# Kernel tuning notes

Measured on AMD Instinct MI355X. Metric: run time of the kernel, lower is better.

## Reference

```python
import jax, jax.numpy as jnp
import numpy as np

D_MODEL = 1024
N_HEADS = 16
D_K = D_MODEL // N_HEADS  # 64
D_FF = 2688
THETA = 10000.0
EPS = 1e-5
B, S = 2, 2048


def _rmsnorm(x, w):
    xf = x.astype(jnp.float32)
    ms = jnp.mean(xf * xf, axis=-1, keepdims=True)
    return (xf * w * jax.lax.rsqrt(ms + EPS)).astype(x.dtype)


def _rope(x, cos, sin):
    # x: [B, S, H, D_K]; cos/sin: [S, D_K//2]
    xe = x[..., 0::2]
    xo = x[..., 1::2]
    c = cos[None, :, None, :]
    s = sin[None, :, None, :]
    re = xe * c - xo * s
    ro = xe * s + xo * c
    # interleave back to even/odd layout
    return jnp.stack([re, ro], axis=-1).reshape(x.shape)


def setup_inputs() -> dict:
    key = jax.random.key(0)
    ks = jax.random.split(key, 12)
    sc = 0.02  # keep activations numerically sane (stand-in for trunc_normal init)
    return {
        "x": jax.random.normal(ks[0], (B, S, D_MODEL), dtype=jnp.float32),
        "ln1_w": jax.random.normal(ks[1], (D_MODEL,), dtype=jnp.float32) * sc + 1.0,
        "q_w": jax.random.normal(ks[2], (D_MODEL, D_MODEL), dtype=jnp.float32) * sc,
        "k_w": jax.random.normal(ks[3], (D_MODEL, D_MODEL), dtype=jnp.float32) * sc,
        "v_w": jax.random.normal(ks[4], (D_MODEL, D_MODEL), dtype=jnp.float32) * sc,
        "o_w": jax.random.normal(ks[5], (D_MODEL, D_MODEL), dtype=jnp.float32) * sc,
        "ln2_w": jax.random.normal(ks[6], (D_MODEL,), dtype=jnp.float32) * sc + 1.0,
        "w1_w": jax.random.normal(ks[7], (D_FF, D_MODEL), dtype=jnp.float32) * sc,
        "w3_w": jax.random.normal(ks[8], (D_FF, D_MODEL), dtype=jnp.float32) * sc,
        "w2_w": jax.random.normal(ks[9], (D_MODEL, D_FF), dtype=jnp.float32) * sc,
        "token_positions": jnp.arange(S, dtype=jnp.int32),
    }


def reference(x, ln1_w, q_w, k_w, v_w, o_w, ln2_w, w1_w, w3_w, w2_w, token_positions):
    b, s, _ = x.shape
    # --- pre-norm attention sublayer ---
    h = _rmsnorm(x, ln1_w)
    Q = (h @ q_w.T).reshape(b, s, N_HEADS, D_K)
    K = (h @ k_w.T).reshape(b, s, N_HEADS, D_K)
    V = (h @ v_w.T).reshape(b, s, N_HEADS, D_K)

    # RoPE tables from token positions
    pos = token_positions.astype(jnp.float32)                      # [S]
    kk = jnp.arange(D_K // 2, dtype=jnp.float32)
    inv_freq = THETA ** (-2.0 * kk / D_K)                          # [D_K/2]
    ang = pos[:, None] * inv_freq[None, :]                          # [S, D_K/2]
    cos, sin = jnp.cos(ang), jnp.sin(ang)

    Qr = _rope(Q, cos, sin)
    Kr = _rope(K, cos, sin)

    scale = 1.0 / jnp.sqrt(jnp.float32(D_K))
    scores = jnp.einsum("bqhd,bkhd->bhqk", Qr, Kr) * scale          # [B,H,S,S]
    causal = jnp.tril(jnp.ones((s, s), dtype=bool))
    scores = jnp.where(causal[None, None], scores, jnp.float32(-10000.0))
    attn = jax.nn.softmax(scores, axis=-1)
    ctx = jnp.einsum("bhqk,bkhd->bqhd", attn, V).reshape(b, s, D_MODEL)
    x1 = x + ctx @ o_w.T

    # --- pre-norm SwiGLU FFN sublayer ---
    h2 = _rmsnorm(x1, ln2_w)
    g = h2 @ w1_w.T                                                 # [B,S,D_FF]
    u = h2 @ w3_w.T
    ffn = (g * jax.nn.sigmoid(g) * u) @ w2_w.T
    return x1 + ffn
```

## Files before the change

kernel.cpp:

```cpp
#include <hip/hip_runtime.h>
#include <cstdint>

#define DM   1024
#define NH   16
#define DK   64
#define DFF  2688
#define SEQ  2048
#define BB   2
#define MTOT (BB*SEQ)

typedef __attribute__((ext_vector_type(8))) short short8;
typedef __attribute__((ext_vector_type(4))) float f32x4;

typedef const __attribute__((address_space(1))) void* gaddr_t;
typedef __attribute__((address_space(3))) void* laddr_t;
#define GLOAD_LDS16(g, l) __builtin_amdgcn_global_load_lds((gaddr_t)(g), (laddr_t)(l), 16, 0, 0)
#define MFMA16(a, b, c) __builtin_amdgcn_mfma_f32_16x16x32_bf16((a), (b), (c), 0, 0, 0)
#define WAIT_LDS() __builtin_amdgcn_s_waitcnt(0xc07f)

__device__ __forceinline__ float bf2f(unsigned short u) {
    union { unsigned int i; float f; } v; v.i = ((unsigned int)u) << 16; return v.f;
}
__device__ __forceinline__ unsigned short f2bf(float f) {
    union { float f; unsigned int i; } v; v.f = f;
    unsigned int r = v.i + 0x7fffu + ((v.i >> 16) & 1u);
    return (unsigned short)(r >> 16);
}
__device__ __forceinline__ unsigned long long pack4bf(float a, float b, float c, float d) {
    return (unsigned long long)f2bf(a) | ((unsigned long long)f2bf(b) << 16)
         | ((unsigned long long)f2bf(c) << 32) | ((unsigned long long)f2bf(d) << 48);
}

__global__ __launch_bounds__(256)
void prep_k(const float* __restrict__ q_w, const float* __restrict__ k_w,
            const float* __restrict__ v_w, const float* __restrict__ o_w,
            const float* __restrict__ w1_w, const float* __restrict__ w3_w,
            const float* __restrict__ w2_w,
            unsigned short* __restrict__ Wqkv, unsigned short* __restrict__ Wo,
            unsigned short* __restrict__ W13, unsigned short* __restrict__ W2) {
    const int blk = blockIdx.x;
    const float* src; unsigned short* dst; int cols, rmul, roff, i;
    if (blk < 4096) {
        const int rr = blk >> 10;
        i = (blk & 1023) * 256 + threadIdx.x;
        cols = 1024; rmul = 1;
        if (rr == 0)      { src = q_w; dst = Wqkv; roff = 0; }
        else if (rr == 1) { src = k_w; dst = Wqkv; roff = 1024; }
        else if (rr == 2) { src = v_w; dst = Wqkv; roff = 2048; }
        else              { src = o_w; dst = Wo;   roff = 0; }
    } else if (blk < 6784) {
        i = (blk - 4096) * 256 + threadIdx.x; src = w1_w; dst = W13; cols = 1024; rmul = 2; roff = 0;
    } else if (blk < 9472) {
        i = (blk - 6784) * 256 + threadIdx.x; src = w3_w; dst = W13; cols = 1024; rmul = 2; roff = 1;
    } else {
        i = (blk - 9472) * 256 + threadIdx.x; src = w2_w; dst = W2;  cols = 2688; rmul = 1; roff = 0;
    }
    const int e = i * 4;
    const int r = e / cols, c = e - r * cols;
    const float4 v = *(const float4*)(src + e);
    ushort4 o;
    o.x = f2bf(v.x); o.y = f2bf(v.y); o.z = f2bf(v.z); o.w = f2bf(v.w);
    *(ushort4*)(dst + (size_t)(r * rmul + roff) * cols + c) = o;
}

__global__ __launch_bounds__(256)
void rmsnorm_k(const float* __restrict__ x, const float* __restrict__ w,
               unsigned short* __restrict__ out) {
    const int row = blockIdx.x;
    const int tid = threadIdx.x;
    const float4 v = ((const float4*)(x + (size_t)row * DM))[tid];
    float ss = v.x * v.x + v.y * v.y + v.z * v.z + v.w * v.w;
#pragma unroll
    for (int off = 32; off > 0; off >>= 1) ss += __shfl_down(ss, off, 64);
    __shared__ float sred[4];
    const int wave = tid >> 6, lane = tid & 63;
    if (lane == 0) sred[wave] = ss;
    __syncthreads();
    const float tot = sred[0] + sred[1] + sred[2] + sred[3];
    const float rinv = rsqrtf(tot * (1.0f / DM) + 1e-5f);
    const float4 wv = ((const float4*)w)[tid];
    ushort4 o;
    o.x = f2bf(v.x * wv.x * rinv);
    o.y = f2bf(v.y * wv.y * rinv);
    o.z = f2bf(v.z * wv.z * rinv);
    o.w = f2bf(v.w * wv.w * rinv);
    ((ushort4*)(out + (size_t)row * DM))[tid] = o;
}

template <int EPI, int TN>
__global__ __launch_bounds__(256)
void gemm_bt(const unsigned short* __restrict__ A,
             const unsigned short* __restrict__ B,
             unsigned short* __restrict__ Cb,
             float* __restrict__ Cf,
             const float* __restrict__ R,
             int N, int K) {
    constexpr int NJ  = (TN == 128) ? 4 : 2;
    constexpr int BPT = (TN == 128) ? 4 : 2;
    __shared__ unsigned short As[8192];
    __shared__ unsigned short Bs[TN * 64];
    const int tid = threadIdx.x;
    const int wave = tid >> 6, lane = tid & 63;
    const int l15 = lane & 15, quad = lane >> 4;
    const int m0 = blockIdx.y * 128, n0 = blockIdx.x * TN;
    const int wr = (TN == 128) ? (wave >> 1) * 64 : (wave & 1) * 64;
    const int wc = (TN == 128) ? (wave & 1) * 64 : (wave >> 1) * 32;

    const f32x4 z4 = {0.f, 0.f, 0.f, 0.f};
    f32x4 acc[4][NJ];
#pragma unroll
    for (int i = 0; i < 4; i++)
#pragma unroll
        for (int j = 0; j < NJ; j++) acc[i][j] = z4;

    const unsigned short* ap[4];
    int albase[4];
#pragma unroll
    for (int i = 0; i < 4; i++) {
        const int s = i * 256 + tid;
        ap[i] = A + (size_t)(m0 + (s & 127)) * K + (s >> 7) * 8;
        albase[i] = (i * 256 + wave * 64) * 8;
    }
    const unsigned short* bp[BPT];
    int blbase[BPT];
#pragma unroll
    for (int i = 0; i < BPT; i++) {
        const int s = i * 256 + tid;
        const int nn = (TN == 128) ? (s & 127) : (s & 63);
        const int k8 = (TN == 128) ? (s >> 7) : (s >> 6);
        bp[i] = B + (size_t)(n0 + nn) * K + k8 * 8;
        blbase[i] = (i * 256 + wave * 64) * 8;
    }

    const int nk = K >> 6;
    for (int kc = 0; kc < nk; kc++) {
        __syncthreads();
#pragma unroll
        for (int i = 0; i < 4; i++) { GLOAD_LDS16(ap[i], &As[albase[i]]); ap[i] += 64; }
#pragma unroll
        for (int i = 0; i < BPT; i++) { GLOAD_LDS16(bp[i], &Bs[blbase[i]]); bp[i] += 64; }
        __syncthreads();
#pragma unroll
        for (int h = 0; h < 2; h++) {
            short8 af[4], bg[NJ];
#pragma unroll
            for (int t = 0; t < 4; t++)
                af[t] = *(const short8*)(&As[((quad + 4 * h) * 128 + wr + t * 16 + l15) * 8]);
#pragma unroll
            for (int t = 0; t < NJ; t++)
                bg[t] = *(const short8*)(&Bs[((quad + 4 * h) * TN + wc + t * 16 + l15) * 8]);
#pragma unroll
            for (int i = 0; i < 4; i++)
#pragma unroll
                for (int j = 0; j < NJ; j++)
                    acc[i][j] = MFMA16(bg[j], af[i], acc[i][j]);
        }
    }

#pragma unroll
    for (int i = 0; i < 4; i++) {
        const int r = m0 + wr + i * 16 + l15;
#pragma unroll
        for (int j = 0; j < NJ; j++) {
            const int cc = n0 + wc + j * 16 + quad * 4;
            const size_t idx = (size_t)r * N + cc;
            if (EPI == 0) {
                *(unsigned long long*)(Cb + idx) =
                    pack4bf(acc[i][j][0], acc[i][j][1], acc[i][j][2], acc[i][j][3]);
            } else {
                const float4 rv = *(const float4*)(R + idx);
                float4 ov;
                ov.x = acc[i][j][0] + rv.x;
                ov.y = acc[i][j][1] + rv.y;
                ov.z = acc[i][j][2] + rv.z;
                ov.w = acc[i][j][3] + rv.w;
                *(float4*)(Cf + idx) = ov;
            }
        }
    }
}

__global__ void rope_tab_k(const int* __restrict__ pos, float* __restrict__ tab) {
    const int s = blockIdx.x, t = threadIdx.x;
    const int kk = t & 31;
    const float ang = (float)pos[s] * __expf(-0.28782313662f * (float)kk);
    tab[s * 64 + t] = (t < 32) ? cosf(ang) : sinf(ang);
}

__global__ __launch_bounds__(256)
void rope_k(const unsigned short* __restrict__ qkv, const float* __restrict__ tab,
            unsigned short* __restrict__ Qr, unsigned short* __restrict__ Kr) {
    const int m = blockIdx.x;
    const int s = m & (SEQ - 1), b = m >> 11;
    const int tid = threadIdx.x;
#pragma unroll
    for (int i = 0; i < 2; i++) {
        const int pr = i * 256 + tid;
        const int h = pr >> 5, k = pr & 31;
        const float cs = tab[s * 64 + k];
        const float sn = tab[s * 64 + 32 + k];
        const size_t so = (size_t)m * 3072 + h * 64 + 2 * k;
        const size_t doff = ((size_t)(b * NH + h) * SEQ + s) * DK + 2 * k;
        const unsigned int q2 = *(const unsigned int*)(qkv + so);
        float xe = bf2f((unsigned short)(q2 & 0xffffu));
        float xo = bf2f((unsigned short)(q2 >> 16));
        *(unsigned int*)(Qr + doff) =
            (unsigned int)f2bf(xe * cs - xo * sn) | ((unsigned int)f2bf(xe * sn + xo * cs) << 16);
        const unsigned int k2 = *(const unsigned int*)(qkv + so + 1024);
        xe = bf2f((unsigned short)(k2 & 0xffffu));
        xo = bf2f((unsigned short)(k2 >> 16));
        *(unsigned int*)(Kr + doff) =
            (unsigned int)f2bf(xe * cs - xo * sn) | ((unsigned int)f2bf(xe * sn + xo * cs) << 16);
    }
}

__global__ __launch_bounds__(256)
void vtrans_k(const unsigned short* __restrict__ qkv, unsigned short* __restrict__ Vt) {
    __shared__ unsigned short tile[64 * 72];
    const int bh = blockIdx.y;
    const int b = bh >> 4, h = bh & 15;
    const int s0 = blockIdx.x * 64;
    const int tid = threadIdx.x;
#pragma unroll
    for (int i = 0; i < 2; i++) {
        const int idx = i * 256 + tid;
        const int sl = idx >> 3, d8 = (idx & 7) * 8;
        const uint4 v = *(const uint4*)(qkv + (size_t)(b * SEQ + s0 + sl) * 3072 + 2048 + h * 64 + d8);
        *(uint4*)(tile + sl * 72 + d8) = v;
    }
    __syncthreads();
#pragma unroll
    for (int i = 0; i < 2; i++) {
        const int idx = i * 256 + tid;
        const int d = idx >> 3, s8 = (idx & 7) * 8;
        unsigned short tmp[8] __attribute__((aligned(16)));
#pragma unroll
        for (int j = 0; j < 8; j++) tmp[j] = tile[(s8 + j) * 72 + d];
        *(uint4*)(Vt + ((size_t)bh * DK + d) * SEQ + s0 + s8) = *(const uint4*)tmp;
    }
}

template <bool MASK>
__device__ __forceinline__ void softmax_tile(f32x4 st[4], float& li, unsigned short* Pw,
                                             int l15, int quad, int j0, int myq) {
    float lsum = 0.f;
#pragma unroll
    for (int t = 0; t < 4; t++) {
#pragma unroll
        for (int r = 0; r < 4; r++) {
            float v = st[t][r] * 0.125f;
            if (MASK) {
                const int key = j0 + t * 16 + quad * 4 + r;
                if (key > myq) v = -1e30f;
            }
            const float p = __expf(v);
            st[t][r] = p;
            lsum += p;
        }
        *(unsigned long long*)(Pw + l15 * 72 + t * 16 + quad * 4) =
            pack4bf(st[t][0], st[t][1], st[t][2], st[t][3]);
    }
    li += lsum;
}

__global__ __launch_bounds__(256, 2)
void attn_k(const unsigned short* __restrict__ Qr, const unsigned short* __restrict__ Kr,
            const unsigned short* __restrict__ Vt, unsigned short* __restrict__ ctx) {
    __shared__ unsigned short KVl[2][8192];
    __shared__ unsigned short Pl[4 * 2 * 1152];
    const int tid = threadIdx.x;
    const int wave = tid >> 6, lane = tid & 63;
    const int l15 = lane & 15, quad = lane >> 4;
    const int bh = blockIdx.y, b = bh >> 4, h = bh & 15;
    const int g = blockIdx.x;
    const int qtA = g * 4 + wave, qtB = 127 - qtA;
    const int q0A = qtA * 16, q0B = qtB * 16;
    const int countA = g + 1, countB = 32 - g;
    const unsigned short* Kb = Kr + (size_t)bh * SEQ * DK;
    const unsigned short* Vb = Vt + (size_t)bh * DK * SEQ;

    const unsigned short* QbA = Qr + ((size_t)bh * SEQ + q0A) * DK;
    const unsigned short* QbB = Qr + ((size_t)bh * SEQ + q0B) * DK;
    const short8 qfA0 = *(const short8*)(QbA + l15 * DK + quad * 8);
    const short8 qfA1 = *(const short8*)(QbA + l15 * DK + 32 + quad * 8);
    const short8 qfB0 = *(const short8*)(QbB + l15 * DK + quad * 8);
    const short8 qfB1 = *(const short8*)(QbB + l15 * DK + 32 + quad * 8);

    const int slot0 = wave * 128 + lane, slot1 = slot0 + 64;
    const int ck0 = slot0 >> 3, s0 = slot0 & 7;
    const int ck1 = slot1 >> 3, s1 = slot1 & 7;
    const unsigned short* kp0 = Kb + ck0 * 64 + (s0 ^ (ck0 & 7)) * 8;
    const unsigned short* kp1 = Kb + ck1 * 64 + (s1 ^ (ck1 & 7)) * 8;
    const unsigned short* vp0 = Vb + ck0 * 2048 + (s0 ^ (ck0 & 7)) * 8;
    const unsigned short* vp1 = Vb + ck1 * 2048 + (s1 ^ (ck1 & 7)) * 8;
    const int kb0 = wave * 1024, kb1 = kb0 + 512;

    unsigned short* PA = Pl + (wave * 2 + 0) * 1152;
    unsigned short* PB = Pl + (wave * 2 + 1) * 1152;

    const f32x4 z4 = {0.f, 0.f, 0.f, 0.f};
    f32x4 oA[4], oB[4];
#pragma unroll
    for (int d = 0; d < 4; d++) { oA[d] = z4; oB[d] = z4; }
    float liA = 0.f, liB = 0.f;
    const int myqA = q0A + l15, myqB = q0B + l15;
    const int xr = l15 & 7;

    GLOAD_LDS16(kp0, &KVl[0][kb0]);
    GLOAD_LDS16(kp1, &KVl[0][kb1]);
    GLOAD_LDS16(vp0, &KVl[0][4096 + kb0]);
    GLOAD_LDS16(vp1, &KVl[0][4096 + kb1]);
    kp0 += 4096; kp1 += 4096; vp0 += 64; vp1 += 64;

    for (int j = 0; j < countB; ++j) {
        const int bf = j & 1;
        const unsigned short* Kl = KVl[bf];
        const unsigned short* Vl = KVl[bf] + 4096;
        __syncthreads();
        if (j + 1 < countB) {
            GLOAD_LDS16(kp0, &KVl[bf ^ 1][kb0]);
            GLOAD_LDS16(kp1, &KVl[bf ^ 1][kb1]);
            GLOAD_LDS16(vp0, &KVl[bf ^ 1][4096 + kb0]);
            GLOAD_LDS16(vp1, &KVl[bf ^ 1][4096 + kb1]);
            kp0 += 4096; kp1 += 4096; vp0 += 64; vp1 += 64;
        }
        const int j0 = j * 64;
        short8 kf[4][2];
#pragma unroll
        for (int t = 0; t < 4; t++) {
            const unsigned short* kr = Kl + (t * 16 + l15) * 64;
            kf[t][0] = *(const short8*)(kr + (quad ^ xr) * 8);
            kf[t][1] = *(const short8*)(kr + ((4 + quad) ^ xr) * 8);
        }
        f32x4 stB[4];
#pragma unroll
        for (int t = 0; t < 4; t++)
            stB[t] = MFMA16(kf[t][1], qfB1, MFMA16(kf[t][0], qfB0, z4));
        const bool doA = (j < countA);
        if (doA) {
            f32x4 stA[4];
#pragma unroll
            for (int t = 0; t < 4; t++)
                stA[t] = MFMA16(kf[t][1], qfA1, MFMA16(kf[t][0], qfA0, z4));
            if (j == countA - 1) softmax_tile<true >(stA, liA, PA, l15, quad, j0, myqA);
            else                 softmax_tile<false>(stA, liA, PA, l15, quad, j0, myqA);
        }
        if (j == countB - 1) softmax_tile<true >(stB, liB, PB, l15, quad, j0, myqB);
        else                 softmax_tile<false>(stB, liB, PB, l15, quad, j0, myqB);
        WAIT_LDS();
        short8 vf[4][2];
#pragma unroll
        for (int dt = 0; dt < 4; dt++) {
            const unsigned short* vr = Vl + (dt * 16 + l15) * 64;
            vf[dt][0] = *(const short8*)(vr + (quad ^ xr) * 8);
            vf[dt][1] = *(const short8*)(vr + ((4 + quad) ^ xr) * 8);
        }
        {
            const short8 pfB0 = *(const short8*)(PB + l15 * 72 + quad * 8);
            const short8 pfB1 = *(const short8*)(PB + l15 * 72 + 32 + quad * 8);
#pragma unroll
            for (int dt = 0; dt < 4; dt++)
                oB[dt] = MFMA16(vf[dt][1], pfB1, MFMA16(vf[dt][0], pfB0, oB[dt]));
        }
        if (doA) {
            const short8 pfA0 = *(const short8*)(PA + l15 * 72 + quad * 8);
            const short8 pfA1 = *(const short8*)(PA + l15 * 72 + 32 + quad * 8);
#pragma unroll
            for (int dt = 0; dt < 4; dt++)
                oA[dt] = MFMA16(vf[dt][1], pfA1, MFMA16(vf[dt][0], pfA0, oA[dt]));
        }
    }
    liA += __shfl_xor(liA, 16, 64); liA += __shfl_xor(liA, 32, 64);
    liB += __shfl_xor(liB, 16, 64); liB += __shfl_xor(liB, 32, 64);
    const float invA = 1.0f / liA, invB = 1.0f / liB;
#pragma unroll
    for (int dt = 0; dt < 4; dt++) {
        *(unsigned long long*)(PA + l15 * 72 + dt * 16 + quad * 4) =
            pack4bf(oA[dt][0] * invA, oA[dt][1] * invA, oA[dt][2] * invA, oA[dt][3] * invA);
        *(unsigned long long*)(PB + l15 * 72 + dt * 16 + quad * 4) =
            pack4bf(oB[dt][0] * invB, oB[dt][1] * invB, oB[dt][2] * invB, oB[dt][3] * invB);
    }
    WAIT_LDS();
    const int row = lane >> 2, seg = (lane & 3) * 8;
#pragma unroll
    for (int p = 0; p < 2; p++) {
        const int cs = seg + p * 32;
        const uint4 va = *(const uint4*)(PA + row * 72 + cs);
        *(uint4*)(ctx + ((size_t)b * SEQ + q0A + row) * DM + h * DK + cs) = va;
        const uint4 vb = *(const uint4*)(PB + row * 72 + cs);
        *(uint4*)(ctx + ((size_t)b * SEQ + q0B + row) * DM + h * DK + cs) = vb;
    }
}

__global__ __launch_bounds__(256)
void silu_k(const unsigned short* __restrict__ gu, unsigned short* __restrict__ act, int npairs) {
    const int i = blockIdx.x * 256 + threadIdx.x;
    const int p0 = i * 4;
    if (p0 >= npairs) return;
    unsigned short in[8] __attribute__((aligned(16)));
    *(uint4*)in = *(const uint4*)(gu + (size_t)p0 * 2);
    unsigned short ov[8] __attribute__((aligned(8)));
#pragma unroll
    for (int j = 0; j < 4; j++) {
        const float g = bf2f(in[2 * j]);
        const float u = bf2f(in[2 * j + 1]);
        ov[j] = f2bf(g * u / (1.f + __expf(-g)));
    }
    *(ushort4*)(act + p0) = *(const ushort4*)ov;
}

extern "C" void kernel_launch(void* const* d_in, const int* in_sizes, int n_in,
                              void* d_out, int out_size, void* d_ws, size_t ws_size,
                              hipStream_t stream) {
    const float* x     = (const float*)d_in[0];
    const float* ln1_w = (const float*)d_in[1];
    const float* q_w   = (const float*)d_in[2];
    const float* k_w   = (const float*)d_in[3];
    const float* v_w   = (const float*)d_in[4];
    const float* o_w   = (const float*)d_in[5];
    const float* ln2_w = (const float*)d_in[6];
    const float* w1_w  = (const float*)d_in[7];
    const float* w3_w  = (const float*)d_in[8];
    const float* w2_w  = (const float*)d_in[9];
    const int*   tpos  = (const int*)d_in[10];
    float* out = (float*)d_out;
    char* ws = (char*)d_ws;

    unsigned short* Wqkv = (unsigned short*)(ws + 0);
    unsigned short* Wo   = (unsigned short*)(ws + 6291456);
    unsigned short* W13  = (unsigned short*)(ws + 8388608);
    unsigned short* W2   = (unsigned short*)(ws + 19398656);
    float*          X1   = (float*)(ws + 24903680);
    float*          ROPT = (float*)(ws + 24903680);
    char* base = ws + 41680896;
    unsigned short* H    = (unsigned short*)(base);
    unsigned short* QKV  = (unsigned short*)(base + 8388608);
    unsigned short* QR   = (unsigned short*)(base + 33554432);
    unsigned short* KR   = (unsigned short*)(base + 41943040);
    unsigned short* VT   = (unsigned short*)(base + 50331648);
    unsigned short* CTX  = (unsigned short*)(base);
    unsigned short* H2   = (unsigned short*)(base + 8388608);
    unsigned short* GU   = (unsigned short*)(base + 16777216);
    unsigned short* ACT  = (unsigned short*)(base + 60817408);

    prep_k<<<12160, 256, 0, stream>>>(q_w, k_w, v_w, o_w, w1_w, w3_w, w2_w,
                                      Wqkv, Wo, W13, W2);
    rope_tab_k<<<2048, 64, 0, stream>>>(tpos, ROPT);

    rmsnorm_k<<<4096, 256, 0, stream>>>(x, ln1_w, H);
    gemm_bt<0,128><<<dim3(24, 32), 256, 0, stream>>>(H, Wqkv, QKV, nullptr, nullptr, 3072, 1024);
    rope_k<<<4096, 256, 0, stream>>>(QKV, ROPT, QR, KR);
    vtrans_k<<<dim3(32, 32), 256, 0, stream>>>(QKV, VT);
    attn_k<<<dim3(16, 32), 256, 0, stream>>>(QR, KR, VT, CTX);
    gemm_bt<1,64><<<dim3(16, 32), 256, 0, stream>>>(CTX, Wo, nullptr, X1, x, 1024, 1024);
    rmsnorm_k<<<4096, 256, 0, stream>>>(X1, ln2_w, H2);
    gemm_bt<0,128><<<dim3(42, 32), 256, 0, stream>>>(H2, W13, GU, nullptr, nullptr, 5376, 1024);
    silu_k<<<10752, 256, 0, stream>>>(GU, ACT, 11010048);
    gemm_bt<1,64><<<dim3(16, 32), 256, 0, stream>>>(ACT, W2, nullptr, out, X1, 1024, 2688);
}
```

Before: 457.5 us.

## Use 256x128 block tiles with K=32 steps for the QKV and W1/W3 GEMMs

```diff
diff --git a/kernel.cpp b/kernel.cpp
--- a/kernel.cpp
+++ b/kernel.cpp
@@ -87,72 +87,156 @@
     ((ushort4*)(out + (size_t)row * DM))[tid] = o;
 }
 
-template <int EPI, int TN>
-__global__ __launch_bounds__(256)
-void gemm_bt(const unsigned short* __restrict__ A,
-             const unsigned short* __restrict__ B,
-             unsigned short* __restrict__ Cb,
-             float* __restrict__ Cf,
-             const float* __restrict__ R,
-             int N, int K) {
-    constexpr int NJ  = (TN == 128) ? 4 : 2;
-    constexpr int BPT = (TN == 128) ? 4 : 2;
+template <int EPI>
+__global__ __launch_bounds__(256)
+void gemm_big(const unsigned short* __restrict__ A,
+              const unsigned short* __restrict__ B,
+              unsigned short* __restrict__ Cb,
+              float* __restrict__ Cf,
+              const float* __restrict__ R,
+              int N, int K) {
     __shared__ unsigned short As[8192];
-    __shared__ unsigned short Bs[TN * 64];
+    __shared__ unsigned short Bs[4096];
     const int tid = threadIdx.x;
     const int wave = tid >> 6, lane = tid & 63;
     const int l15 = lane & 15, quad = lane >> 4;
-    const int m0 = blockIdx.y * 128, n0 = blockIdx.x * TN;
-    const int wr = (TN == 128) ? (wave >> 1) * 64 : (wave & 1) * 64;
-    const int wc = (TN == 128) ? (wave & 1) * 64 : (wave >> 1) * 32;
+    const int m0 = blockIdx.y * 256, n0 = blockIdx.x * 128;
+    const int wr = (wave >> 1) * 128, wc = (wave & 1) * 64;
 
     const f32x4 z4 = {0.f, 0.f, 0.f, 0.f};
-    f32x4 acc[4][NJ];
+    f32x4 acc[8][4];
+#pragma unroll
+    for (int i = 0; i < 8; i++)
+#pragma unroll
+        for (int j = 0; j < 4; j++) acc[i][j] = z4;
+
+    const unsigned short* ap[4];
+    int al[4];
+#pragma unroll
+    for (int i = 0; i < 4; i++) {
+        const int s = i * 256 + tid;
+        ap[i] = A + (size_t)(m0 + (s & 255)) * K + (s >> 8) * 8;
+        al[i] = (i * 256 + wave * 64) * 8;
+    }
+    const unsigned short* bp[2];
+    int bl[2];
+#pragma unroll
+    for (int i = 0; i < 2; i++) {
+        const int s = i * 256 + tid;
+        bp[i] = B + (size_t)(n0 + (s & 127)) * K + (s >> 7) * 8;
+        bl[i] = (i * 256 + wave * 64) * 8;
+    }
+
+    const int nk = K >> 5;
+    for (int kc = 0; kc < nk; kc++) {
+        __syncthreads();
+#pragma unroll
+        for (int i = 0; i < 4; i++) { GLOAD_LDS16(ap[i], &As[al[i]]); ap[i] += 32; }
+#pragma unroll
+        for (int i = 0; i < 2; i++) { GLOAD_LDS16(bp[i], &Bs[bl[i]]); bp[i] += 32; }
+        __syncthreads();
+        short8 bg[4];
+#pragma unroll
+        for (int j = 0; j < 4; j++)
+            bg[j] = *(const short8*)(&Bs[(quad * 128 + wc + j * 16 + l15) * 8]);
+#pragma unroll
+        for (int h = 0; h < 2; h++) {
+            short8 af[4];
+#pragma unroll
+            for (int t = 0; t < 4; t++)
+                af[t] = *(const short8*)(&As[(quad * 256 + wr + h * 64 + t * 16 + l15) * 8]);
+#pragma unroll
+            for (int t = 0; t < 4; t++)
+#pragma unroll
+                for (int j = 0; j < 4; j++)
+                    acc[h * 4 + t][j] = MFMA16(bg[j], af[t], acc[h * 4 + t][j]);
+        }
+    }
+
+#pragma unroll
+    for (int i = 0; i < 8; i++) {
+        const int r = m0 + wr + i * 16 + l15;
+#pragma unroll
+        for (int j = 0; j < 4; j++) {
+            const int cc = n0 + wc + j * 16 + quad * 4;
+            const size_t idx = (size_t)r * N + cc;
+            if (EPI == 0) {
+                *(unsigned long long*)(Cb + idx) =
+                    pack4bf(acc[i][j][0], acc[i][j][1], acc[i][j][2], acc[i][j][3]);
+            } else {
+                const float4 rv = *(const float4*)(R + idx);
+                float4 ov;
+                ov.x = acc[i][j][0] + rv.x;
+                ov.y = acc[i][j][1] + rv.y;
+                ov.z = acc[i][j][2] + rv.z;
+                ov.w = acc[i][j][3] + rv.w;
+                *(float4*)(Cf + idx) = ov;
+            }
+        }
+    }
+}
+
+template <int EPI>
+__global__ __launch_bounds__(256)
+void gemm_thin(const unsigned short* __restrict__ A,
+               const unsigned short* __restrict__ B,
+               unsigned short* __restrict__ Cb,
+               float* __restrict__ Cf,
+               const float* __restrict__ R,
+               int N, int K) {
+    __shared__ unsigned short As[8192];
+    __shared__ unsigned short Bs[4096];
+    const int tid = threadIdx.x;
+    const int wave = tid >> 6, lane = tid & 63;
+    const int l15 = lane & 15, quad = lane >> 4;
+    const int m0 = blockIdx.y * 128, n0 = blockIdx.x * 64;
+    const int wr = (wave & 1) * 64, wc = (wave >> 1) * 32;
+
+    const f32x4 z4 = {0.f, 0.f, 0.f, 0.f};
+    f32x4 acc[4][2];
 #pragma unroll
     for (int i = 0; i < 4; i++)
 #pragma unroll
-        for (int j = 0; j < NJ; j++) acc[i][j] = z4;
+        for (int j = 0; j < 2; j++) acc[i][j] = z4;
 
     const unsigned short* ap[4];
-    int albase[4];
+    int al[4];
 #pragma unroll
     for (int i = 0; i < 4; i++) {
         const int s = i * 256 + tid;
         ap[i] = A + (size_t)(m0 + (s & 127)) * K + (s >> 7) * 8;
-        albase[i] = (i * 256 + wave * 64) * 8;
-    }
-    const unsigned short* bp[BPT];
-    int blbase[BPT];
-#pragma unroll
-    for (int i = 0; i < BPT; i++) {
+        al[i] = (i * 256 + wave * 64) * 8;
+    }
+    const unsigned short* bp[2];
+    int bl[2];
+#pragma unroll
+    for (int i = 0; i < 2; i++) {
         const int s = i * 256 + tid;
-        const int nn = (TN == 128) ? (s & 127) : (s & 63);
-        const int k8 = (TN == 128) ? (s >> 7) : (s >> 6);
-        bp[i] = B + (size_t)(n0 + nn) * K + k8 * 8;
-        blbase[i] = (i * 256 + wave * 64) * 8;
+        bp[i] = B + (size_t)(n0 + (s & 63)) * K + (s >> 6) * 8;
+        bl[i] = (i * 256 + wave * 64) * 8;
     }
 
     const int nk = K >> 6;
     for (int kc = 0; kc < nk; kc++) {
         __syncthreads();
 #pragma unroll
-        for (int i = 0; i < 4; i++) { GLOAD_LDS16(ap[i], &As[albase[i]]); ap[i] += 64; }
-#pragma unroll
-        for (int i = 0; i < BPT; i++) { GLOAD_LDS16(bp[i], &Bs[blbase[i]]); bp[i] += 64; }
+        for (int i = 0; i < 4; i++) { GLOAD_LDS16(ap[i], &As[al[i]]); ap[i] += 64; }
+#pragma unroll
+        for (int i = 0; i < 2; i++) { GLOAD_LDS16(bp[i], &Bs[bl[i]]); bp[i] += 64; }
         __syncthreads();
 #pragma unroll
         for (int h = 0; h < 2; h++) {
-            short8 af[4], bg[NJ];
+            short8 af[4], bg[2];
 #pragma unroll
             for (int t = 0; t < 4; t++)
                 af[t] = *(const short8*)(&As[((quad + 4 * h) * 128 + wr + t * 16 + l15) * 8]);
 #pragma unroll
-            for (int t = 0; t < NJ; t++)
-                bg[t] = *(const short8*)(&Bs[((quad + 4 * h) * TN + wc + t * 16 + l15) * 8]);
+            for (int t = 0; t < 2; t++)
+                bg[t] = *(const short8*)(&Bs[((quad + 4 * h) * 64 + wc + t * 16 + l15) * 8]);
 #pragma unroll
             for (int i = 0; i < 4; i++)
 #pragma unroll
-                for (int j = 0; j < NJ; j++)
+                for (int j = 0; j < 2; j++)
                     acc[i][j] = MFMA16(bg[j], af[i], acc[i][j]);
         }
     }
@@ -161,7 +245,7 @@
     for (int i = 0; i < 4; i++) {
         const int r = m0 + wr + i * 16 + l15;
 #pragma unroll
-        for (int j = 0; j < NJ; j++) {
+        for (int j = 0; j < 2; j++) {
             const int cc = n0 + wc + j * 16 + quad * 4;
             const size_t idx = (size_t)r * N + cc;
             if (EPI == 0) {
@@ -448,13 +532,13 @@
     rope_tab_k<<<2048, 64, 0, stream>>>(tpos, ROPT);
 
     rmsnorm_k<<<4096, 256, 0, stream>>>(x, ln1_w, H);
-    gemm_bt<0,128><<<dim3(24, 32), 256, 0, stream>>>(H, Wqkv, QKV, nullptr, nullptr, 3072, 1024);
+    gemm_big<0><<<dim3(24, 16), 256, 0, stream>>>(H, Wqkv, QKV, nullptr, nullptr, 3072, 1024);
     rope_k<<<4096, 256, 0, stream>>>(QKV, ROPT, QR, KR);
     vtrans_k<<<dim3(32, 32), 256, 0, stream>>>(QKV, VT);
     attn_k<<<dim3(16, 32), 256, 0, stream>>>(QR, KR, VT, CTX);
-    gemm_bt<1,64><<<dim3(16, 32), 256, 0, stream>>>(CTX, Wo, nullptr, X1, x, 1024, 1024);
+    gemm_thin<1><<<dim3(16, 32), 256, 0, stream>>>(CTX, Wo, nullptr, X1, x, 1024, 1024);
     rmsnorm_k<<<4096, 256, 0, stream>>>(X1, ln2_w, H2);
-    gemm_bt<0,128><<<dim3(42, 32), 256, 0, stream>>>(H2, W13, GU, nullptr, nullptr, 5376, 1024);
+    gemm_big<0><<<dim3(42, 16), 256, 0, stream>>>(H2, W13, GU, nullptr, nullptr, 5376, 1024);
     silu_k<<<10752, 256, 0, stream>>>(GU, ACT, 11010048);
-    gemm_bt<1,64><<<dim3(16, 32), 256, 0, stream>>>(ACT, W2, nullptr, out, X1, 1024, 2688);
-}
+    gemm_thin<1><<<dim3(16, 32), 256, 0, stream>>>(ACT, W2, nullptr, out, X1, 1024, 2688);
+}
```

After: 566.6 us. 23.8% more time.
